# Kernel tuning notes

Hardware: AMD Instinct MI355X
Metric: run time of the kernel (lower is better)

## Reference

```python
import jax, jax.numpy as jnp
import numpy as np

B, S, DIN, DOUT = 4, 2048, 4096, 4096

def setup_inputs() -> dict:
    key = jax.random.key(0)
    k1, k2, k3 = jax.random.split(key, 3)
    inp = jax.random.normal(k1, (B, S, DIN), dtype=jnp.float16)
    # int8 quantized weights in [-127, 127]
    qweight = jax.random.randint(k2, (DOUT, DIN), -127, 128, dtype=jnp.int32).astype(jnp.int8)
    # per-output-channel scales, small positive
    qscales = (jax.random.uniform(k3, (DOUT, 1), dtype=jnp.float32) * 0.01 + 1e-4).astype(jnp.float16)
    return {"inp": inp, "qweight": qweight, "qscales": qscales}

def reference(inp, qweight, qscales):
    # Dequantize: int8 * fp16 scale -> fp16 weight [out, in] (matches torch promotion + .to(fp16))
    w = (qweight.astype(jnp.float16) * qscales).astype(jnp.float16)
    # F.linear(inp, w) = inp @ w.T ; note: bias is NOT added in the original forward
    return jnp.einsum("bsd,od->bso", inp, w)
```

## Files before the change

kernel.cpp:

```cpp
#include <hip/hip_runtime.h>
#include <stdint.h>


#define M_DIM 8192
#define N_DIM 4096
#define K_DIM 4096
#define BM 256
#define BN 256
#define BK 64
#define NKT (K_DIM / BK)

typedef _Float16 f16;
typedef f16 f16x8 __attribute__((ext_vector_type(8)));
typedef f16 f16x2 __attribute__((ext_vector_type(2)));
typedef float f32x4 __attribute__((ext_vector_type(4)));

static __device__ __forceinline__ f16x2 cvt2(float a, float b) {
  return __builtin_bit_cast(f16x2, __builtin_amdgcn_cvt_pkrtz(a, b));
}


__global__ __launch_bounds__(256) void conv_a_kernel(
    const float* __restrict__ A, f16* __restrict__ Af)
{
  const size_t stride = (size_t)gridDim.x * blockDim.x;
  size_t i = (size_t)blockIdx.x * blockDim.x + threadIdx.x;
  const size_t n8 = (size_t)M_DIM * K_DIM / 8;
  for (; i < n8; i += stride) {
    const f32x4* p = (const f32x4*)(A + i * 8);
    f32x4 v0 = p[0], v1 = p[1];
    f16x2 a = cvt2(v0.x, v0.y), b = cvt2(v0.z, v0.w);
    f16x2 c = cvt2(v1.x, v1.y), d = cvt2(v1.z, v1.w);
    *(f16x8*)(Af + i * 8) = (f16x8){a.x, a.y, b.x, b.y, c.x, c.y, d.x, d.y};
  }
}

__global__ __launch_bounds__(256) void conv_b_kernel(
    const int* __restrict__ Qw, const float* __restrict__ Sc,
    f16* __restrict__ Wf)
{
  const int o = blockIdx.x;
  const int t = threadIdx.x;
  const float s = Sc[o];
  const int* q = Qw + (size_t)o * K_DIM + t * 16;
  f16* w = Wf + (size_t)o * K_DIM + t * 16;
  #pragma unroll
  for (int h = 0; h < 2; ++h) {
    int4 u0 = *(const int4*)(q + h * 8);
    int4 u1 = *(const int4*)(q + h * 8 + 4);
    f16x2 a = cvt2((float)u0.x * s, (float)u0.y * s);
    f16x2 b = cvt2((float)u0.z * s, (float)u0.w * s);
    f16x2 c = cvt2((float)u1.x * s, (float)u1.y * s);
    f16x2 d = cvt2((float)u1.z * s, (float)u1.w * s);
    *(f16x8*)(w + h * 8) = (f16x8){a.x, a.y, b.x, b.y, c.x, c.y, d.x, d.y};
  }
}


#define BARX() __builtin_amdgcn_s_barrier()
#define LGKM0() do { asm volatile("s_waitcnt lgkmcnt(0)" ::: "memory"); \
                     __builtin_amdgcn_sched_barrier(0); } while (0)
#define VMW(n) asm volatile("s_waitcnt vmcnt(" #n ")" ::: "memory")

#define LOADA(buf, qm) do { \
  const char* _b = (const char*)&As[buf][qm][0]; \
  _Pragma("unroll") \
  for (int j = 0; j < 4; ++j) { \
    const int _lr = (2 * j + wm) * 16 + fr; \
    af[j][0] = *(const f16x8*)(_b + _lr * 128 + (((qk    ) ^ x7) << 4)); \
    af[j][1] = *(const f16x8*)(_b + _lr * 128 + (((qk + 4) ^ x7) << 4)); \
  } } while (0)

#define LOADB(buf, qn, bf) do { \
  const char* _b = (const char*)&Bs[buf][qn][0]; \
  _Pragma("unroll") \
  for (int nl = 0; nl < 2; ++nl) { \
    const int _lr = nl * 64 + wn * 16 + fr; \
    bf[nl][0] = *(const f16x8*)(_b + _lr * 128 + (((qk    ) ^ x7) << 4)); \
    bf[nl][1] = *(const f16x8*)(_b + _lr * 128 + (((qk + 4) ^ x7) << 4)); \
  } } while (0)

#define MFMAQ(qm, qn, bf) do { \
  __builtin_amdgcn_s_setprio(1); \
  _Pragma("unroll") \
  for (int j = 0; j < 4; ++j) \
    _Pragma("unroll") \
    for (int nl = 0; nl < 2; ++nl) { \
      acc[(qm)*4 + j][(qn)*2 + nl] = __builtin_amdgcn_mfma_f32_16x16x32_f16( \
          af[j][0], bf[nl][0], acc[(qm)*4 + j][(qn)*2 + nl], 0, 0, 0); \
      acc[(qm)*4 + j][(qn)*2 + nl] = __builtin_amdgcn_mfma_f32_16x16x32_f16( \
          af[j][1], bf[nl][1], acc[(qm)*4 + j][(qn)*2 + nl], 0, 0, 0); \
    } \
  __builtin_amdgcn_s_setprio(0); } while (0)

#define STAGE(dstHalf, srcPanel, h, ktn) do { \
  _Pragma("unroll") \
  for (int _i = 0; _i < 2; ++_i) { \
    const f16* _g = (srcPanel) + (size_t)((h) * 128 + _i * 64 + st_row) * K_DIM \
                    + (ktn) * 64 + st_slot * 8; \
    char* _l = (char*)(dstHalf) + _i * 8192 + wid * 1024; \
    __builtin_amdgcn_global_load_lds( \
        (const __attribute__((address_space(1))) void*)_g, \
        (__attribute__((address_space(3))) void*)_l, 16, 0, 0); \
  } } while (0)

__global__ __launch_bounds__(512) void w8a16_gemm_f16_kernel(
    const f16* __restrict__ Af,
    const f16* __restrict__ Wf,
    float* __restrict__ Out)
{
  __shared__ __align__(16) f16 As[2][2][128 * 64];
  __shared__ __align__(16) f16 Bs[2][2][128 * 64];

  const int t    = threadIdx.x;
  const int lane = t & 63;
  const int wid  = t >> 6;
  const int wm   = wid >> 2;
  const int wn   = wid & 3;
  const int fr   = lane & 15;
  const int qk   = lane >> 4;
  const int x7   = fr & 7;

  const int st_row  = t >> 3;
  const int st_slot = (t & 7) ^ ((t >> 3) & 7);

  const int bid = blockIdx.x;
  const int swz = (bid & 7) * 64 + (bid >> 3);
  const int tn  = swz & 15;
  const int tm  = swz >> 4;

  const f16* aSrc = Af + (size_t)tm * BM * K_DIM;
  const f16* bSrc = Wf + (size_t)tn * BN * K_DIM;

  f32x4 acc[8][4] = {};
  f16x8 af[4][2], bf0[2][2], bf1[2][2];

  STAGE(&As[0][0][0], aSrc, 0, 0);
  STAGE(&Bs[0][0][0], bSrc, 0, 0);
  STAGE(&Bs[0][1][0], bSrc, 1, 0);
  STAGE(&As[0][1][0], aSrc, 1, 0);
  VMW(2);
  BARX();

  for (int kt = 0; kt < NKT; ++kt) {
    const int  buf  = kt & 1;
    const int  nbuf = buf ^ 1;
    const bool more = (kt + 1) < NKT;

    LOADA(buf, 0);
    LOADB(buf, 0, bf0);
    if (more) STAGE(&As[nbuf][0][0], aSrc, 0, kt + 1);
    BARX(); LGKM0();
    MFMAQ(0, 0, bf0);
    BARX();

    LOADB(buf, 1, bf1);
    if (more) { STAGE(&Bs[nbuf][0][0], bSrc, 0, kt + 1); VMW(4); }
    else      { VMW(0); }
    BARX(); LGKM0();
    MFMAQ(0, 1, bf1);
    BARX();

    LOADA(buf, 1);
    if (more) STAGE(&Bs[nbuf][1][0], bSrc, 1, kt + 1);
    BARX(); LGKM0();
    MFMAQ(1, 1, bf1);
    BARX();

    if (more) { STAGE(&As[nbuf][1][0], aSrc, 1, kt + 1); VMW(2); }
    BARX(); LGKM0();
    MFMAQ(1, 0, bf0);
    BARX();
  }

  const int fq = lane >> 4;
  #pragma unroll
  for (int mi = 0; mi < 8; ++mi) {
    const size_t row = (size_t)tm * BM + (mi * 2 + wm) * 16 + fq * 4;
    #pragma unroll
    for (int ni = 0; ni < 4; ++ni) {
      const size_t col = (size_t)tn * BN + ni * 64 + wn * 16 + fr;
      #pragma unroll
      for (int r = 0; r < 4; ++r)
        Out[(row + r) * N_DIM + col] = acc[mi][ni][r];
    }
  }
}


__global__ __launch_bounds__(256) void w8a16_gemm_fb_kernel(
    const float* __restrict__ A, const int* __restrict__ Qw,
    const float* __restrict__ Sc, float* __restrict__ Out)
{
  __shared__ __align__(16) float Asf[2][128 * 32];
  __shared__ __align__(16) f16 Bsf[2][128][32];

  const int t = threadIdx.x, lane = t & 63, wid = t >> 6;
  const int wr = wid >> 1, wc = wid & 1;
  const int nwg = gridDim.x, cpx = nwg >> 3, bid = blockIdx.x;
  const int swz = (bid & 7) * cpx + (bid >> 3);
  const int tn = swz & 31, tm = swz >> 5;
  const size_t a_base = (size_t)tm * 128 * K_DIM;
  const size_t b_base = (size_t)tn * 128 * K_DIM;
  f32x4 acc[4][4] = {};
  const int a_r = t >> 3;
  const int a_slog = (t & 7) ^ ((t >> 3) & 7);

  auto stageA = [&](int buf, int kt) {
    #pragma unroll
    for (int c = 0; c < 4; ++c) {
      const float* g = A + a_base + (size_t)(c * 32 + a_r) * K_DIM + kt * 32 + a_slog * 4;
      char* l = (char*)&Asf[buf][0] + c * 4096 + wid * 1024;
      __builtin_amdgcn_global_load_lds(
          (const __attribute__((address_space(1))) void*)g,
          (__attribute__((address_space(3))) void*)l, 16, 0, 0);
    }
  };
  const int b_r = t >> 3, b_col = (t & 7) * 4;
  auto loadB = [&](int kt, int4* v) {
    #pragma unroll
    for (int c = 0; c < 4; ++c)
      v[c] = *(const int4*)(Qw + b_base + (size_t)(c * 32 + b_r) * K_DIM + kt * 32 + b_col);
  };
  auto writeB = [&](int buf, const int4* v) {
    #pragma unroll
    for (int c = 0; c < 4; ++c) {
      f16x2 lo = cvt2((float)v[c].x, (float)v[c].y);
      f16x2 hi = cvt2((float)v[c].z, (float)v[c].w);
      *(f16x2*)&Bsf[buf][c * 32 + b_r][b_col] = lo;
      *(f16x2*)&Bsf[buf][c * 32 + b_r][b_col + 2] = hi;
    }
  };
  auto compute = [&](int buf) {
    const int fr2 = lane & 15, q = lane >> 4;
    f16x8 af2[4], bf2[4];
    #pragma unroll
    for (int i = 0; i < 4; ++i) {
      const int r = wr * 64 + i * 16 + fr2;
      const float* base = &Asf[buf][0] + r * 32;
      const int s0 = q * 2;
      f32x4 a0 = *(const f32x4*)(base + ((s0 ^ (r & 7)) * 4));
      f32x4 a1 = *(const f32x4*)(base + (((s0 + 1) ^ (r & 7)) * 4));
      f16x2 p0 = cvt2(a0.x, a0.y), p1 = cvt2(a0.z, a0.w);
      f16x2 p2 = cvt2(a1.x, a1.y), p3 = cvt2(a1.z, a1.w);
      af2[i] = (f16x8){p0.x, p0.y, p1.x, p1.y, p2.x, p2.y, p3.x, p3.y};
      bf2[i] = *(const f16x8*)&Bsf[buf][wc * 64 + i * 16 + fr2][q * 8];
    }
    #pragma unroll
    for (int mi = 0; mi < 4; ++mi)
      #pragma unroll
      for (int ni = 0; ni < 4; ++ni)
        acc[mi][ni] = __builtin_amdgcn_mfma_f32_16x16x32_f16(
            af2[mi], bf2[ni], acc[mi][ni], 0, 0, 0);
  };

  { int4 b0[4]; stageA(0, 0); loadB(0, b0); writeB(0, b0); }
  __syncthreads();
  for (int kt = 0; kt < K_DIM / 32; ++kt) {
    const int buf = kt & 1;
    const bool more = (kt + 1) < K_DIM / 32;
    int4 nb[4];
    if (more) { stageA(buf ^ 1, kt + 1); loadB(kt + 1, nb); }
    compute(buf);
    if (more) writeB(buf ^ 1, nb);
    __syncthreads();
  }
  const int fr2 = lane & 15, fq = lane >> 4;
  const int cb = tn * 128 + wc * 64 + fr2;
  const int rb = tm * 128 + wr * 64 + fq * 4;
  #pragma unroll
  for (int ni = 0; ni < 4; ++ni) {
    const float s = Sc[cb + ni * 16];
    #pragma unroll
    for (int mi = 0; mi < 4; ++mi)
      #pragma unroll
      for (int r = 0; r < 4; ++r)
        Out[(size_t)(rb + mi * 16 + r) * N_DIM + (cb + ni * 16)] =
            acc[mi][ni][r] * s;
  }
}

extern "C" void kernel_launch(void* const* d_in, const int* in_sizes, int n_in,
                              void* d_out, int out_size, void* d_ws, size_t ws_size,
                              hipStream_t stream) {
  const float* A  = (const float*)d_in[0];
  const int*   Qw = (const int*)d_in[1];
  const float* Sc = (const float*)d_in[2];
  float*       Out = (float*)d_out;

  const size_t a_bytes = (size_t)M_DIM * K_DIM * sizeof(f16);
  const size_t w_bytes = (size_t)N_DIM * K_DIM * sizeof(f16);

  if (ws_size >= a_bytes + w_bytes) {
    f16* Af = (f16*)d_ws;
    f16* Wf = (f16*)((char*)d_ws + a_bytes);
    conv_a_kernel<<<2048, 256, 0, stream>>>(A, Af);
    conv_b_kernel<<<N_DIM, 256, 0, stream>>>(Qw, Sc, Wf);
    dim3 grid((M_DIM / BM) * (N_DIM / BN));
    w8a16_gemm_f16_kernel<<<grid, 512, 0, stream>>>(Af, Wf, Out);
  } else {
    dim3 grid((M_DIM / 128) * (N_DIM / 128));
    w8a16_gemm_fb_kernel<<<grid, 256, 0, stream>>>(A, Qw, Sc, Out);
  }
}
```

Baseline: 305.4 us.

## Deepen global-to-LDS prefetch pipeline with unrolled two-tile main loop

Restructures the GEMM main loop into a two-K-tile unrolled schedule with fixed buffer indices. Loads for the next tile are issued further ahead: three quarters of tile kt+1 are preloaded in the prologue, and within each step the remaining panels are staged earlier with relaxed vmcnt/lgkmcnt waits and sched barriers. The aim is to hide global-load latency better behind MFMA work. It also adds launch_bounds min-blocks 1 and an explicit epilogue for the last two tiles. The cost is more code and tighter ordering assumptions between LDS reuse and the barriers.

```diff
diff --git a/kernel.cpp b/kernel.cpp
--- a/kernel.cpp
+++ b/kernel.cpp
@@ -58,8 +58,10 @@
 
 
 #define BARX() __builtin_amdgcn_s_barrier()
+#define SCHED0() __builtin_amdgcn_sched_barrier(0)
 #define LGKM0() do { asm volatile("s_waitcnt lgkmcnt(0)" ::: "memory"); \
                      __builtin_amdgcn_sched_barrier(0); } while (0)
+#define LGKM8() asm volatile("s_waitcnt lgkmcnt(8)" ::: "memory")
 #define VMW(n) asm volatile("s_waitcnt vmcnt(" #n ")" ::: "memory")
 
 #define LOADA(buf, qm) do { \
@@ -104,7 +106,7 @@
         (__attribute__((address_space(3))) void*)_l, 16, 0, 0); \
   } } while (0)
 
-__global__ __launch_bounds__(512) void w8a16_gemm_f16_kernel(
+__global__ __launch_bounds__(512, 1) void w8a16_gemm_f16_kernel(
     const f16* __restrict__ Af,
     const f16* __restrict__ Wf,
     float* __restrict__ Out)
@@ -139,38 +141,101 @@
   STAGE(&Bs[0][0][0], bSrc, 0, 0);
   STAGE(&Bs[0][1][0], bSrc, 1, 0);
   STAGE(&As[0][1][0], aSrc, 1, 0);
-  VMW(2);
+  STAGE(&As[1][0][0], aSrc, 0, 1);
+  STAGE(&Bs[1][0][0], bSrc, 0, 1);
+  STAGE(&Bs[1][1][0], bSrc, 1, 1);
+  VMW(6);
   BARX();
-
-  for (int kt = 0; kt < NKT; ++kt) {
-    const int  buf  = kt & 1;
-    const int  nbuf = buf ^ 1;
-    const bool more = (kt + 1) < NKT;
-
-    LOADA(buf, 0);
-    LOADB(buf, 0, bf0);
-    if (more) STAGE(&As[nbuf][0][0], aSrc, 0, kt + 1);
+  SCHED0();
+
+  for (int kt = 0; kt < NKT - 2; kt += 2) {
+    LOADA(0, 0);
+    LOADB(0, 0, bf0);
+    STAGE(&As[1][1][0], aSrc, 1, kt + 1);
+    LGKM8();
     BARX(); LGKM0();
     MFMAQ(0, 0, bf0);
     BARX();
-
-    LOADB(buf, 1, bf1);
-    if (more) { STAGE(&Bs[nbuf][0][0], bSrc, 0, kt + 1); VMW(4); }
-    else      { VMW(0); }
+    LOADB(0, 1, bf1);
+    STAGE(&As[0][0][0], aSrc, 0, kt + 2);
     BARX(); LGKM0();
     MFMAQ(0, 1, bf1);
     BARX();
-
-    LOADA(buf, 1);
-    if (more) STAGE(&Bs[nbuf][1][0], bSrc, 1, kt + 1);
+    LOADA(0, 1);
+    STAGE(&Bs[0][0][0], bSrc, 0, kt + 2);
     BARX(); LGKM0();
     MFMAQ(1, 1, bf1);
     BARX();
-
-    if (more) { STAGE(&As[nbuf][1][0], aSrc, 1, kt + 1); VMW(2); }
-    BARX(); LGKM0();
+    STAGE(&Bs[0][1][0], bSrc, 1, kt + 2);
+    VMW(6);
+    BARX();
     MFMAQ(1, 0, bf0);
     BARX();
+    LOADA(1, 0);
+    LOADB(1, 0, bf0);
+    STAGE(&As[0][1][0], aSrc, 1, kt + 2);
+    LGKM8();
+    BARX(); LGKM0();
+    MFMAQ(0, 0, bf0);
+    BARX();
+    LOADB(1, 1, bf1);
+    STAGE(&As[1][0][0], aSrc, 0, kt + 3);
+    BARX(); LGKM0();
+    MFMAQ(0, 1, bf1);
+    BARX();
+    LOADA(1, 1);
+    STAGE(&Bs[1][0][0], bSrc, 0, kt + 3);
+    BARX(); LGKM0();
+    MFMAQ(1, 1, bf1);
+    BARX();
+    STAGE(&Bs[1][1][0], bSrc, 1, kt + 3);
+    VMW(6);
+    BARX();
+    MFMAQ(1, 0, bf0);
+    BARX();
+  }
+
+  {
+    LOADA(0, 0);
+    LOADB(0, 0, bf0);
+    STAGE(&As[1][1][0], aSrc, 1, NKT - 1);
+    LGKM8();
+    BARX(); LGKM0();
+    MFMAQ(0, 0, bf0);
+    BARX();
+
+    LOADB(0, 1, bf1);
+    BARX(); LGKM0();
+    MFMAQ(0, 1, bf1);
+    BARX();
+
+    LOADA(0, 1);
+    BARX(); LGKM0();
+    MFMAQ(1, 1, bf1);
+    BARX();
+
+    VMW(0);
+    BARX();
+    MFMAQ(1, 0, bf0);
+    BARX();
+
+    LOADA(1, 0);
+    LOADB(1, 0, bf0);
+    BARX(); LGKM0();
+    MFMAQ(0, 0, bf0);
+    BARX();
+
+    LOADB(1, 1, bf1);
+    BARX(); LGKM0();
+    MFMAQ(0, 1, bf1);
+    BARX();
+
+    LOADA(1, 1);
+    BARX(); LGKM0();
+    MFMAQ(1, 1, bf1);
+    BARX();
+
+    MFMAQ(1, 0, bf0);
   }
 
   const int fq = lane >> 4;
```

After: 299.9 us. Within noise of the previous version (-1.8%).
